# Performance work log

Measured on AMD Instinct MI355X. Metric: run time of the kernel, lower is better.

Reference implementation:

```python
import jax, jax.numpy as jnp
import numpy as np

B, T, HID = 2, 2048, 1024
NH = 8
QK_DIM = 1024
V_DIM = 2048
SCALE_BASE = 512.0
GN_EPS = 1e-5


def _xpos_rotate(x, downscale):
    # x: [B, T, QK_DIM]; XPOS rotary embedding (syncdoth/RetNet, offset=0)
    d = QK_DIM
    dh = d // 2
    pos = jnp.arange(T, dtype=jnp.float32)
    # per-pair magnitude scale
    base_scale = (jnp.arange(0, d, 2, dtype=jnp.float32) + 0.4 * d) / (1.4 * d)  # [dh]
    scale = base_scale[None, :] ** (pos[:, None] / SCALE_BASE)  # [T, dh]
    if downscale:
        scale = 1.0 / scale
    inv_freq = 1.0 / (10000.0 ** (jnp.arange(dh, dtype=jnp.float32) / dh))
    sinusoid = pos[:, None] * inv_freq[None, :]  # [T, dh]
    sin = jnp.sin(sinusoid) * scale
    cos = jnp.cos(sinusoid) * scale
    # duplicate_interleave -> [T, d]
    sin = jnp.repeat(sin, 2, axis=-1)
    cos = jnp.repeat(cos, 2, axis=-1)
    x1 = x[..., 0::2]
    x2 = x[..., 1::2]
    rot = jnp.stack((-x2, x1), axis=-1).reshape(x.shape)  # rotate_every_two
    return x * cos[None] + rot * sin[None]


def setup_inputs() -> dict:
    key = jax.random.key(0)
    k1, k2, k3, k4 = jax.random.split(key, 4)
    x = jax.random.normal(k1, (B, T, HID), dtype=jnp.float32)
    Wqkv = jax.random.normal(k2, (HID, 2 * QK_DIM + V_DIM), dtype=jnp.float32) / np.sqrt(HID)
    Wg = jax.random.normal(k3, (HID, V_DIM), dtype=jnp.float32) / np.sqrt(HID)
    Wp = jax.random.normal(k4, (V_DIM, HID), dtype=jnp.float32) / np.sqrt(V_DIM)
    bp = jnp.zeros((HID,), dtype=jnp.float32)
    return {"x": x, "Wqkv": Wqkv, "Wg": Wg, "Wp": Wp, "bp": bp}


def reference(x, Wqkv, Wg, Wp, bp):
    # multi-scale decay (non-default gamma path)
    gamma = 1.0 - jnp.exp(jnp.linspace(np.log(1.0 / 32), np.log(1.0 / 512), NH)).astype(jnp.float32)  # [NH]

    qkv = x @ Wqkv  # [B,T,2qk+v]
    q, k, v = jnp.split(qkv, [QK_DIM, 2 * QK_DIM], axis=-1)
    q = _xpos_rotate(q, downscale=False)
    k = _xpos_rotate(k, downscale=True)

    dqk = QK_DIM // NH
    dv = V_DIM // NH
    q = q.reshape(B, T, NH, dqk).transpose(0, 2, 1, 3)  # [B,H,T,dqk]
    k = k.reshape(B, T, NH, dqk).transpose(0, 2, 1, 3)
    v = v.reshape(B, T, NH, dv).transpose(0, 2, 1, 3)   # [B,H,T,dv]

    # parallel decay mask: gamma^(i-j) for i>=j else 0  -> [H,T,T]
    idx = jnp.arange(T)
    expo = idx[:, None] - idx[None, :]
    expo_safe = jnp.where(expo >= 0, expo, 0).astype(jnp.float32)
    decay_mask = jnp.where(expo[None] >= 0, gamma[:, None, None] ** expo_safe[None], 0.0)  # [H,T,T]

    scores = jnp.einsum('bhid,bhjd->bhij', q, k) * (dqk ** -0.5)
    retention = jnp.einsum('bhij,bhjv->bhiv', scores * decay_mask[None], v)  # [B,H,T,dv]

    # current_kv state: sum_t decay_mask[h,-1,t] * k_t (outer) v_t  -> [B,H,dqk,dv]
    curr_kv = jnp.einsum('bhtk,bhtv,ht->bhkv', k, v, decay_mask[:, -1, :])

    ret = retention.transpose(0, 2, 1, 3).reshape(B, T, V_DIM)

    # GroupNorm(num_groups=NH, affine=False) over [B*T, V_DIM]
    g = ret.reshape(B, T, NH, dv)
    mu = jnp.mean(g, axis=-1, keepdims=True)
    var = jnp.var(g, axis=-1, keepdims=True)
    normed = ((g - mu) / jnp.sqrt(var + GN_EPS)).reshape(B, T, V_DIM)

    gate = jax.nn.silu(x @ Wg)
    out = (gate * normed) @ Wp + bp
    return out, curr_kv
```

## Files before the change

kernel.cpp:

```cpp
#include <hip/hip_runtime.h>

typedef unsigned short u16;
typedef unsigned int   u32;
typedef unsigned long long u64;

typedef __attribute__((ext_vector_type(8))) short bf8_t;
typedef __attribute__((ext_vector_type(4))) float f4_t;

#define DEVI __device__ __forceinline__
#define MFMA16(a,b,c) __builtin_amdgcn_mfma_f32_16x16x32_bf16((a),(b),(c),0,0,0)

#define BB   2
#define TT   2048
#define HIDN 1024
#define L0f  (-3.4657359027997265f)
#define DLf  (-0.3960841031714215f)
#define SCL  (0.08838834764831845f)

DEVI u16 f2b(float f) {
    u32 u = __float_as_uint(f);
    u += 0x7FFFu + ((u >> 16) & 1u);
    return (u16)(u >> 16);
}
DEVI float b2f(u16 u) { return __uint_as_float(((u32)u) << 16); }

DEVI void gll16(const void* g, void* l) {
    __builtin_amdgcn_global_load_lds((const __attribute__((address_space(1))) void*)g,
                                     (__attribute__((address_space(3))) void*)l, 16, 0, 0);
}

__global__ __launch_bounds__(256) void k_tables(u32* __restrict__ cqp, u32* __restrict__ ckp,
                                                float* __restrict__ gt, float* __restrict__ gk) {
    int bx = blockIdx.x;
    if (bx >= 4096) {
        int i = (bx - 4096) * 256 + threadIdx.x;
        if (i < 16384) {
            int h = i >> 11, t = i & 2047;
            float lg2 = log2f(1.f - expf(L0f + (float)h * DLf));
            gt[i] = exp2f((float)(2047 - t) * lg2);
        } else {
            int idx = i - 16384;
            int h = idx >> 6, d = idx & 63;
            float lg2 = log2f(1.f - expf(L0f + (float)h * DLf));
            gk[idx] = exp2f(-(float)d * lg2);
        }
        return;
    }
    int idx = bx * 256 + threadIdx.x;
    int t = idx >> 9, m = idx & 511;
    float base = (2.f * (float)m + 409.6f) * (1.f / 1433.6f);
    float s = exp2f(log2f(base) * ((float)t * (1.f / 512.f)));
    float invf = exp2f(-(float)m * (13.287712379549449f / 512.f));
    float sn, cs;
    sincosf((float)t * invf, &sn, &cs);
    int h = m >> 6;
    float lg2h = log2f(1.f - expf(L0f + (float)h * DLf));
    float qf = s * SCL * exp2f((float)(t & 63) * lg2h);
    cqp[idx] = (u32)f2b(cs * qf) | ((u32)f2b(sn * qf) << 16);
    float is = 1.f / s;
    ckp[idx] = (u32)f2b(cs * is) | ((u32)f2b(sn * is) << 16);
}

__global__ __launch_bounds__(256) void k_cvt(const float* __restrict__ in, u16* __restrict__ out) {
    int i = blockIdx.x * 256 + threadIdx.x;
    float4 v = ((const float4*)in)[i];
    u64 pk = (u64)f2b(v.x) | ((u64)f2b(v.y) << 16) | ((u64)f2b(v.z) << 32) | ((u64)f2b(v.w) << 48);
    ((u64*)out)[i] = pk;
}

__global__ __launch_bounds__(256) void k_tposeF(const float* __restrict__ Wqkv,
                                                const float* __restrict__ Wg,
                                                const float* __restrict__ Wp,
                                                u16* __restrict__ oQ, u16* __restrict__ oG,
                                                u16* __restrict__ oP) {
    __shared__ float tile[32][33];
    int bx = blockIdx.x;
    const float* in; u16* out; int R, C, cx, ry;
    if (bx < 4096)      { in = Wqkv; out = oQ; R = 1024; C = 4096; cx = bx & 127;        ry = bx >> 7; }
    else if (bx < 6144) { int b2 = bx - 4096; in = Wg; out = oG; R = 1024; C = 2048; cx = b2 & 63; ry = b2 >> 6; }
    else                { int b2 = bx - 6144; in = Wp; out = oP; R = 2048; C = 1024; cx = b2 & 31; ry = b2 >> 5; }
    int c0 = cx * 32, r0 = ry * 32;
    int tx = threadIdx.x, ty = threadIdx.y;
#pragma unroll
    for (int i = 0; i < 4; i++)
        tile[ty * 4 + i][tx] = in[(size_t)(r0 + ty * 4 + i) * C + c0 + tx];
    __syncthreads();
#pragma unroll
    for (int i = 0; i < 4; i++)
        out[(size_t)(c0 + ty * 4 + i) * R + r0 + tx] = f2b(tile[tx][ty * 4 + i]);
}

DEVI void stage_tile(const u16* __restrict__ A, const u16* __restrict__ B,
                     int m0, int n0, int kt, char* buf, int tid, int wid) {
#pragma unroll
    for (int q = 0; q < 4; q++) {
        int flat = q * 8192 + tid * 16;
        int row = flat >> 7, byt = (flat & 127) ^ ((row & 7) << 4);
        gll16((const char*)A + (size_t)(m0 + row) * 2048 + kt * 128 + byt,
              buf + q * 8192 + wid * 1024);
        gll16((const char*)B + (size_t)(n0 + row) * 2048 + kt * 128 + byt,
              buf + 32768 + q * 8192 + wid * 1024);
    }
}

#define QPHASE(kk, fmh, LOADB)                                                        \
    {                                                                                 \
        bf8_t a_[4];                                                                  \
        _Pragma("unroll")                                                             \
        for (int f = 0; f < 4; f++) {                                                 \
            int ra = 128 * wr + ((fmh) * 4 + f) * 16 + lr;                            \
            a_[f] = *(const bf8_t*)(bA + ra * 128 + (((kk) * 64 + lg * 16) ^ ((ra & 7) << 4))); \
        }                                                                             \
        if (LOADB) {                                                                  \
            _Pragma("unroll")                                                         \
            for (int f = 0; f < 4; f++) {                                             \
                int rb = 64 * wc + f * 16 + lr;                                       \
                breg[f] = *(const bf8_t*)(bB + rb * 128 + (((kk) * 64 + lg * 16) ^ ((rb & 7) << 4))); \
            }                                                                         \
        }                                                                             \
        __builtin_amdgcn_s_barrier();                                                 \
        __builtin_amdgcn_s_setprio(1);                                                \
        _Pragma("unroll")                                                             \
        for (int f = 0; f < 4; f++)                                                   \
            _Pragma("unroll")                                                         \
            for (int j = 0; j < 4; j++)                                               \
                acc[(fmh) * 4 + f][j] = MFMA16(a_[f], breg[j], acc[(fmh) * 4 + f][j]); \
        __builtin_amdgcn_s_setprio(0);                                                \
        __builtin_amdgcn_s_barrier();                                                 \
    }

__global__ __launch_bounds__(512, 2) void k_gemm_qkvg8(
    const u16* __restrict__ xb, const u16* __restrict__ Wcat,
    const u32* __restrict__ cqp, const u32* __restrict__ ckp, const float* __restrict__ gkt,
    u16* __restrict__ qw, u16* __restrict__ kw, u16* __restrict__ kT, u16* __restrict__ vT,
    u16* __restrict__ gateb) {
    __shared__ __align__(16) char L[131072];
    int flat = blockIdx.x;
    int swz = (flat & 7) * 48 + (flat >> 3);
    int m0 = (swz / 24) * 256, n0 = (swz % 24) * 256;
    int tid = threadIdx.x, lane = tid & 63, wid = tid >> 6;
    int wr = wid >> 2, wc = wid & 3, lr = lane & 15, lg = lane >> 4;
    f4_t acc[8][4];
#pragma unroll
    for (int i = 0; i < 8; i++)
#pragma unroll
        for (int j = 0; j < 4; j++)
#pragma unroll
            for (int e = 0; e < 4; e++) acc[i][j][e] = 0.f;
    stage_tile(xb, Wcat, m0, n0, 0, L, tid, wid);
    __syncthreads();
    for (int kt = 0; kt < 16; ++kt) {
        const char* bA = L + (kt & 1) * 65536;
        const char* bB = bA + 32768;
        if (kt < 15) stage_tile(xb, Wcat, m0, n0, kt + 1, L + ((kt + 1) & 1) * 65536, tid, wid);
        bf8_t breg[4];
        QPHASE(0, 0, 1)
        QPHASE(0, 1, 0)
        QPHASE(1, 0, 1)
        QPHASE(1, 1, 0)
        __syncthreads();
    }
    char* SP = L;
    int b = m0 >> 11, t0 = m0 & 2047;
    if (n0 < 4096 && n0 >= 2048) {
        int h = (n0 - 2048) >> 8;
#pragma unroll
        for (int fm = 0; fm < 8; fm++)
#pragma unroll
            for (int fn = 0; fn < 4; fn++) {
                int dv = wc * 64 + fn * 16 + lr;
                int rowb = wr * 128 + fm * 16 + lg * 4;
                u64 pk = 0;
#pragma unroll
                for (int r = 0; r < 4; r++) pk |= ((u64)f2b(acc[fm][fn][r])) << (16 * r);
                *(u64*)(SP + dv * 512 + ((rowb * 2) ^ ((dv & 15) << 4))) = pk;
            }
        __syncthreads();
#pragma unroll
        for (int it = 0; it < 16; it++) {
            int chunk = it * 512 + tid;
            int dv = chunk >> 5, j = chunk & 31;
            uint4 v = *(const uint4*)(SP + dv * 512 + ((j * 16) ^ ((dv & 15) << 4)));
            *(uint4*)(vT + ((size_t)((b * 8 + h) * 256 + dv)) * 2048 + t0 + j * 8) = v;
        }
    } else if (n0 < 2048) {
        int isK = n0 >= 1024;
        const u32* cT = isK ? ckp : cqp;
        int hb = (n0 >> 7) & 7;
#pragma unroll
        for (int fm = 0; fm < 8; fm++)
#pragma unroll
            for (int fn = 0; fn < 4; fn++) {
                int col = wc * 64 + fn * 16 + lr;
                int gq = (n0 & 1023) + col;
                int mi = gq >> 1, h = gq >> 7;
                u64 pk = 0;
#pragma unroll
                for (int r = 0; r < 4; r++) {
                    int rowl = wr * 128 + fm * 16 + lg * 4 + r;
                    int t = t0 + rowl;
                    float v = acc[fm][fn][r];
                    float pv = __shfl_xor(v, 1);
                    u32 cp = cT[t * 512 + mi];
                    float cs = b2f((u16)cp), sn = b2f((u16)(cp >> 16));
                    float o = (col & 1) ? (v * cs + pv * sn) : (v * cs - pv * sn);
                    if (isK) {
                        pk |= ((u64)f2b(o)) << (16 * r);
                        o *= gkt[h * 64 + (t & 63)];
                    }
                    *(u16*)(SP + rowl * 512 + ((col * 2) ^ ((rowl & 15) << 4))) = f2b(o);
                }
                if (isK)
                    *(u64*)&kT[((size_t)((b * 8 + h) * 128 + (gq & 127))) * 2048 + t0 + wr * 128 + fm * 16 + lg * 4] = pk;
            }
        __syncthreads();
#pragma unroll
        for (int it = 0; it < 16; it++) {
            int chunk = it * 512 + tid;
            int r = chunk >> 5, j = chunk & 31;
            uint4 v = *(const uint4*)(SP + r * 512 + ((j * 16) ^ ((r & 15) << 4)));
            int hh = hb + (j >> 4);
            u16* g = (isK ? kw : qw) + ((size_t)((b * 8 + hh) * 2048 + t0 + r)) * 128 + (j & 15) * 8;
            *(uint4*)g = v;
        }
    } else {
        int c0 = n0 - 4096;
#pragma unroll
        for (int fm = 0; fm < 8; fm++)
#pragma unroll
            for (int fn = 0; fn < 4; fn++) {
                int col = wc * 64 + fn * 16 + lr;
#pragma unroll
                for (int r = 0; r < 4; r++) {
                    int rowl = wr * 128 + fm * 16 + lg * 4 + r;
                    float gg = acc[fm][fn][r];
                    *(u16*)(SP + rowl * 512 + ((col * 2) ^ ((rowl & 15) << 4))) = f2b(gg / (1.f + expf(-gg)));
                }
            }
        __syncthreads();
#pragma unroll
        for (int it = 0; it < 16; it++) {
            int chunk = it * 512 + tid;
            int r = chunk >> 5, j = chunk & 31;
            uint4 v = *(const uint4*)(SP + r * 512 + ((j * 16) ^ ((r & 15) << 4)));
            *(uint4*)(gateb + (size_t)(b * 2048 + t0 + r) * 2048 + c0 + j * 8) = v;
        }
    }
}

DEVI void gemm_ml(const u16* __restrict__ Ag, const u16* __restrict__ Bg, int Klen, int Kstr,
                  int m0, int n0, u16* As, u16* Bs, f4_t acc[4][4]) {
    int tid = threadIdx.x, lane = tid & 63, wid = tid >> 6;
    int wr = wid >> 1, wc = wid & 1, lr = lane & 15, lg = lane >> 4;
    for (int k0 = 0; k0 < Klen; k0 += 64) {
        __syncthreads();
#pragma unroll
        for (int p = 0; p < 4; p++) {
            int flat = p * 4096 + tid * 16;
            int row = flat >> 7, byt = (flat & 127) ^ ((row & 7) << 4);
            gll16((const char*)Ag + ((size_t)(m0 + row) * Kstr + k0) * 2 + byt,
                  (char*)As + p * 4096 + wid * 1024);
            gll16((const char*)Bg + ((size_t)(n0 + row) * Kstr + k0) * 2 + byt,
                  (char*)Bs + p * 4096 + wid * 1024);
        }
        __syncthreads();
#pragma unroll
        for (int kk = 0; kk < 2; kk++) {
            bf8_t a[4], b[4];
#pragma unroll
            for (int f = 0; f < 4; f++) {
                int ra = wr * 64 + f * 16 + lr;
                a[f] = *(const bf8_t*)((const char*)As + ra * 128 + ((kk * 64 + lg * 16) ^ ((ra & 7) << 4)));
                int rb = wc * 64 + f * 16 + lr;
                b[f] = *(const bf8_t*)((const char*)Bs + rb * 128 + ((kk * 64 + lg * 16) ^ ((rb & 7) << 4)));
            }
#pragma unroll
            for (int i = 0; i < 4; i++)
#pragma unroll
                for (int j = 0; j < 4; j++)
                    acc[i][j] = MFMA16(a[i], b[j], acc[i][j]);
        }
    }
}

DEVI void acc_zero(f4_t acc[4][4]) {
#pragma unroll
    for (int i = 0; i < 4; i++)
#pragma unroll
        for (int j = 0; j < 4; j++)
#pragma unroll
            for (int e = 0; e < 4; e++) acc[i][j][e] = 0.f;
}

__global__ __launch_bounds__(256) void k_gemm_outp(const u16* __restrict__ gdb, const u16* __restrict__ Wt,
                                                   float* __restrict__ part) {
    __shared__ u16 SM[128 * 128];
    f4_t acc[4][4]; acc_zero(acc);
    int m0 = blockIdx.y * 128, n0 = blockIdx.x * 128, kz = blockIdx.z;
    gemm_ml(gdb + kz * 1024, Wt + kz * 1024, 1024, 2048, m0, n0, SM, SM + 128 * 64, acc);
    int tid = threadIdx.x, lane = tid & 63, wid = tid >> 6;
    int wr = wid >> 1, wc = wid & 1, lr = lane & 15, lg = lane >> 4;
    float* SMf = (float*)SM;
    float* po = part + (size_t)kz * 4096 * 1024;
    __syncthreads();
#pragma unroll
    for (int p = 0; p < 2; p++) {
        if (p) __syncthreads();
        if (wr == p) {
#pragma unroll
            for (int fm = 0; fm < 4; fm++)
#pragma unroll
                for (int fn = 0; fn < 4; fn++) {
                    int col = wc * 64 + fn * 16 + lr;
#pragma unroll
                    for (int r = 0; r < 4; r++) {
                        int rowl = fm * 16 + lg * 4 + r;
                        *(float*)((char*)SMf + rowl * 512 + ((col * 4) ^ ((rowl & 7) << 6))) = acc[fm][fn][r];
                    }
                }
        }
        __syncthreads();
#pragma unroll
        for (int it2 = 0; it2 < 8; it2++) {
            int chunk = it2 * 256 + tid;
            int rowl = chunk >> 5, j = chunk & 31;
            f4_t v = *(const f4_t*)((const char*)SMf + rowl * 512 + ((j * 16) ^ ((rowl & 7) << 6)));
            *(f4_t*)((char*)po + ((size_t)(m0 + p * 64 + rowl) * 1024 + n0) * 4 + j * 16) = v;
        }
    }
}

__global__ __launch_bounds__(256) void k_outred(const float* __restrict__ part, const float* __restrict__ bp,
                                                float* __restrict__ outp) {
    int i = blockIdx.x * 256 + threadIdx.x;
    f4_t a = ((const f4_t*)part)[i];
    f4_t c = ((const f4_t*)(part + (size_t)4096 * 1024))[i];
    f4_t bb = *(const f4_t*)(bp + ((i * 4) & 1023));
#pragma unroll
    for (int e = 0; e < 4; e++) a[e] += c[e] + bb[e];
    ((f4_t*)outp)[i] = a;
}

__global__ __launch_bounds__(256, 3) void k_retention(const u16* __restrict__ qws, const u16* __restrict__ kws,
                                                      const u16* __restrict__ vTws,
                                                      u16* __restrict__ ret0, u16* __restrict__ ret1) {
    __shared__ u16 SMr[64 * 128 + 256 * 64];
    u16* Ks = SMr;
    u16* Vs = SMr + 64 * 128;
    int x = blockIdx.x;
    int it, jlo, jhi, toret1;
    if (x < 16)      { it = 15 - x;  jlo = 0;              jhi = it + 1;         toret1 = 0; }
    else if (x < 32) { it = x;       jlo = 0;              jhi = (it + 2) >> 1;  toret1 = 0; }
    else             { it = x - 16;  jlo = (it + 2) >> 1;  jhi = it + 1;         toret1 = 1; }
    int h = blockIdx.y, b = blockIdx.z;
    int bh = b * 8 + h;
    float lg2 = log2f(1.f - expf(L0f + (float)h * DLf));
    int i0 = it * 64;
    const u16* qbase = qws + (size_t)bh * 2048 * 128;
    const u16* kbase = kws + (size_t)bh * 2048 * 128;
    const u16* vbase = vTws + (size_t)bh * 256 * 2048;
    int tid = threadIdx.x, lane = tid & 63, w = tid >> 6, lr = lane & 15, lg = lane >> 4;
    bf8_t aq[4];
#pragma unroll
    for (int kk = 0; kk < 4; kk++)
        aq[kk] = *(const bf8_t*)((const char*)qbase + (size_t)(i0 + w * 16 + lr) * 256 + kk * 64 + lg * 16);
    f4_t racc[16];
#pragma unroll
    for (int f = 0; f < 16; f++)
#pragma unroll
        for (int e = 0; e < 4; e++) racc[f][e] = 0.f;
    for (int jt = jlo; jt < jhi; jt++) {
        int j0 = jt * 64;
        int diag = (jt == it);
        float tf = exp2f(64.f * (float)(it - jt) * lg2);
        __syncthreads();
#pragma unroll
        for (int p = 0; p < 4; p++) {
            int flat = p * 4096 + tid * 16;
            int row = flat >> 8, byt = (flat & 255) ^ ((row & 7) << 4);
            gll16((const char*)kbase + (size_t)(j0 + row) * 256 + byt, (char*)Ks + p * 4096 + w * 1024);
        }
#pragma unroll
        for (int p = 0; p < 8; p++) {
            int flat = p * 4096 + tid * 16;
            int row = flat >> 7, byt = (flat & 127) ^ ((row & 7) << 4);
            gll16((const char*)vbase + (size_t)row * 4096 + (size_t)j0 * 2 + byt,
                  (char*)Vs + p * 4096 + w * 1024);
        }
        __syncthreads();
        f4_t sacc[4];
#pragma unroll
        for (int f = 0; f < 4; f++)
#pragma unroll
            for (int e = 0; e < 4; e++) sacc[f][e] = 0.f;
#pragma unroll
        for (int kk = 0; kk < 4; kk++)
#pragma unroll
            for (int fn = 0; fn < 4; fn++) {
                int rb = fn * 16 + lr;
                bf8_t bb = *(const bf8_t*)((const char*)Ks + rb * 256 + ((kk * 64 + lg * 16) ^ ((rb & 7) << 4)));
                sacc[fn] = MFMA16(aq[kk], bb, sacc[fn]);
            }
        __syncthreads();
#pragma unroll
        for (int fn = 0; fn < 4; fn++)
#pragma unroll
            for (int r = 0; r < 4; r++) {
                int i_loc = w * 16 + lg * 4 + r;
                int col = fn * 16 + lr;
                float v = diag ? ((i_loc - col >= 0) ? sacc[fn][r] : 0.f) : sacc[fn][r] * tf;
                *(u16*)((char*)Ks + i_loc * 128 + ((col * 2) ^ ((i_loc & 7) << 4))) = f2b(v);
            }
#pragma unroll
        for (int kk = 0; kk < 2; kk++) {
            int ra = w * 16 + lr;
            bf8_t ap = *(const bf8_t*)((const char*)Ks + ra * 128 + ((kk * 64 + lg * 16) ^ ((ra & 7) << 4)));
#pragma unroll
            for (int fn2 = 0; fn2 < 16; fn2++) {
                int rb = fn2 * 16 + lr;
                bf8_t bv = *(const bf8_t*)((const char*)Vs + rb * 128 + ((kk * 64 + lg * 16) ^ ((rb & 7) << 4)));
                racc[fn2] = MFMA16(ap, bv, racc[fn2]);
            }
        }
    }
    __syncthreads();
    u16* St = Vs;
#pragma unroll
    for (int fn2 = 0; fn2 < 16; fn2++)
#pragma unroll
        for (int r = 0; r < 4; r++) {
            int il = w * 16 + lg * 4 + r;
            int dv = fn2 * 16 + lr;
            *(u16*)((char*)St + il * 512 + ((dv * 2) ^ ((il & 15) << 4))) = f2b(racc[fn2][r]);
        }
    __syncthreads();
#pragma unroll
    for (int it2 = 0; it2 < 8; it2++) {
        int chunk = it2 * 256 + tid;
        int il = chunk >> 5, j = chunk & 31;
        uint4 v = *(const uint4*)((const char*)St + il * 512 + ((j * 16) ^ ((il & 15) << 4)));
        char* dst;
        if (toret1) dst = (char*)ret1 + ((size_t)(b * 1024 + i0 - 1024 + il) * 2048 + h * 256) * 2 + j * 16;
        else        dst = (char*)ret0 + ((size_t)(b * 2048 + i0 + il) * 2048 + h * 256) * 2 + j * 16;
        *(uint4*)dst = v;
    }
}

__global__ __launch_bounds__(512) void k_currkv(const u16* __restrict__ kTws, const u16* __restrict__ vTws,
                                                const float* __restrict__ gtab, float* __restrict__ part) {
    __shared__ u16 Ks2[128 * 64];
    __shared__ u16 Vws[256 * 64];
    int tr = blockIdx.x;
    int bh = blockIdx.y;
    int h = bh & 7;
    const u16* kT = kTws + (size_t)bh * 128 * 2048;
    const u16* vT = vTws + (size_t)bh * 256 * 2048;
    const float* gt = gtab + h * 2048;
    int tid = threadIdx.x, lane = tid & 63, wid = tid >> 6;
    int wr = wid >> 2, wc = wid & 3, lr = lane & 15, lg = lane >> 4;
    f4_t acc[4][4]; acc_zero(acc);
    for (int tc = 0; tc < 8; tc++) {
        int t0 = tr * 512 + tc * 64;
        __syncthreads();
#pragma unroll
        for (int p = 0; p < 2; p++) {
            int flat = p * 8192 + tid * 16;
            int row = flat >> 7, byt = (flat & 127) ^ ((row & 7) << 4);
            gll16((const char*)kT + (size_t)row * 4096 + (size_t)t0 * 2 + byt,
                  (char*)Ks2 + p * 8192 + wid * 1024);
        }
#pragma unroll
        for (int p = 0; p < 4; p++) {
            int flat = p * 8192 + tid * 16;
            int row = flat >> 7, byt = flat & 127;
            int tt = t0 + (byt >> 1);
            const u16* src = vT + (size_t)row * 2048 + tt;
            u16 tmp[8]; *(uint4*)tmp = *(const uint4*)src;
            const float* gp = gt + tt;
            u16 op[8];
#pragma unroll
            for (int e = 0; e < 8; e++) op[e] = f2b(b2f(tmp[e]) * gp[e]);
            *(uint4*)((char*)Vws + row * 128 + (byt ^ ((row & 7) << 4))) = *(uint4*)op;
        }
        __syncthreads();
#pragma unroll
        for (int kk = 0; kk < 2; kk++) {
            bf8_t a[4], bb[4];
#pragma unroll
            for (int f = 0; f < 4; f++) {
                int ra = wr * 64 + f * 16 + lr;
                a[f] = *(const bf8_t*)((const char*)Ks2 + ra * 128 + ((kk * 64 + lg * 16) ^ ((ra & 7) << 4)));
                int rb = wc * 64 + f * 16 + lr;
                bb[f] = *(const bf8_t*)((const char*)Vws + rb * 128 + ((kk * 64 + lg * 16) ^ ((rb & 7) << 4)));
            }
#pragma unroll
            for (int i = 0; i < 4; i++)
#pragma unroll
                for (int j = 0; j < 4; j++)
                    acc[i][j] = MFMA16(a[i], bb[j], acc[i][j]);
        }
    }
#pragma unroll
    for (int fm = 0; fm < 4; fm++)
#pragma unroll
        for (int fn = 0; fn < 4; fn++)
#pragma unroll
            for (int r = 0; r < 4; r++) {
                int dk = wr * 64 + fm * 16 + lg * 4 + r;
                int dv = wc * 64 + fn * 16 + lr;
                part[((size_t)(bh * 4 + tr)) * 32768 + (size_t)dk * 256 + dv] = acc[fm][fn][r];
            }
}

__global__ __launch_bounds__(256) void k_reduce_ckv(const float* __restrict__ part, float* __restrict__ outc) {
    int i = blockIdx.x * 256 + threadIdx.x;
    int bh = i >> 15, wv = i & 32767;
    float s = 0.f;
#pragma unroll
    for (int tr = 0; tr < 4; tr++) s += part[((size_t)(bh * 4 + tr)) * 32768 + wv];
    outc[i] = s;
}

__global__ __launch_bounds__(256) void k_gnorm(const u16* __restrict__ ret0, const u16* __restrict__ ret1,
                                               const u16* __restrict__ gateb, u16* __restrict__ gatedb) {
    int g = blockIdx.x * 4 + (threadIdx.x >> 6);
    int lane = threadIdx.x & 63;
    int row = g >> 3, h = g & 7;
    size_t base = (size_t)row * 2048 + h * 256 + lane * 4;
    u64 p0 = *(const u64*)(ret0 + base);
    float e0 = b2f((u16)p0), e1 = b2f((u16)(p0 >> 16)), e2 = b2f((u16)(p0 >> 32)), e3 = b2f((u16)(p0 >> 48));
    if ((row & 2047) >= 1024) {
        size_t b1 = (size_t)((row >> 11) * 1024 + (row & 1023)) * 2048 + h * 256 + lane * 4;
        u64 p1 = *(const u64*)(ret1 + b1);
        e0 += b2f((u16)p1); e1 += b2f((u16)(p1 >> 16)); e2 += b2f((u16)(p1 >> 32)); e3 += b2f((u16)(p1 >> 48));
    }
    float s = e0 + e1 + e2 + e3;
    float sqs = e0 * e0 + e1 * e1 + e2 * e2 + e3 * e3;
#pragma unroll
    for (int m = 1; m < 64; m <<= 1) { s += __shfl_xor(s, m); sqs += __shfl_xor(sqs, m); }
    float mean = s * (1.f / 256.f);
    float var = sqs * (1.f / 256.f) - mean * mean;
    float inv = rsqrtf(var + 1e-5f);
    u64 gp = *(const u64*)(gateb + base);
    u64 pk = (u64)f2b((e0 - mean) * inv * b2f((u16)gp)) |
             ((u64)f2b((e1 - mean) * inv * b2f((u16)(gp >> 16))) << 16) |
             ((u64)f2b((e2 - mean) * inv * b2f((u16)(gp >> 32))) << 32) |
             ((u64)f2b((e3 - mean) * inv * b2f((u16)(gp >> 48))) << 48);
    *(u64*)(gatedb + base) = pk;
}

extern "C" void kernel_launch(void* const* d_in, const int* in_sizes, int n_in,
                              void* d_out, int out_size, void* d_ws, size_t ws_size,
                              hipStream_t stream) {
    const float* x    = (const float*)d_in[0];
    const float* Wqkv = (const float*)d_in[1];
    const float* Wg   = (const float*)d_in[2];
    const float* Wp   = (const float*)d_in[3];
    const float* bp   = (const float*)d_in[4];
    float* outp   = (float*)d_out;
    float* outckv = outp + (size_t)BB * TT * HIDN;

    char* ws = (char*)d_ws;
    const size_t MB = 1024 * 1024;
    u16*   xb     = (u16*)(ws);
    u16*   WqkvT  = (u16*)(ws + 8 * MB);
    u16*   WgT    = (u16*)(ws + 16 * MB);
    u16*   WpT    = (u16*)(ws + 20 * MB);
    u32*   cqp    = (u32*)(ws + 24 * MB);
    u32*   ckp    = (u32*)(ws + 28 * MB);
    u16*   gateb  = (u16*)(ws + 32 * MB);
    u16*   qw     = (u16*)(ws + 48 * MB);
    u16*   kw     = (u16*)(ws + 56 * MB);
    u16*   kT     = (u16*)(ws + 64 * MB);
    u16*   vT     = (u16*)(ws + 72 * MB);
    u16*   ret0b  = (u16*)(ws + 88 * MB);
    u16*   ret1b  = (u16*)(ws + 104 * MB);
    float* ckvp   = (float*)(ws + 112 * MB);
    float* gtab   = (float*)(ws + 120 * MB);
    float* gkt    = (float*)(ws + 120 * MB + 65536);
    u16*   gatedb = (u16*)(ws + 48 * MB);
    float* opart  = (float*)(ws + 88 * MB);

    hipLaunchKernelGGL(k_tables, dim3(4162), dim3(256), 0, stream, cqp, ckp, gtab, gkt);
    hipLaunchKernelGGL(k_cvt, dim3(4096), dim3(256), 0, stream, x, xb);
    hipLaunchKernelGGL(k_tposeF, dim3(8192), dim3(32, 8), 0, stream, Wqkv, Wg, Wp, WqkvT, WgT, WpT);
    hipLaunchKernelGGL(k_gemm_qkvg8, dim3(384), dim3(512), 0, stream,
                       xb, WqkvT, cqp, ckp, gkt, qw, kw, kT, vT, gateb);
    hipLaunchKernelGGL(k_currkv, dim3(4, 16), dim3(512), 0, stream, kT, vT, gtab, ckvp);
    hipLaunchKernelGGL(k_reduce_ckv, dim3(2048), dim3(256), 0, stream, ckvp, outckv);
    hipLaunchKernelGGL(k_retention, dim3(48, 8, 2), dim3(256), 0, stream, qw, kw, vT, ret0b, ret1b);
    hipLaunchKernelGGL(k_gnorm, dim3(8192), dim3(256), 0, stream, ret0b, ret1b, gateb, gatedb);
    hipLaunchKernelGGL(k_gemm_outp, dim3(8, 32, 2), dim3(256), 0, stream, gatedb, WpT, opart);
    hipLaunchKernelGGL(k_outred, dim3(4096), dim3(256), 0, stream, opart, bp, outp);
}
```

Measured before the change: 225.4 us.

## Halve QKVG GEMM K-tile to 32 to cut LDS and raise occupancy

The fused QKV/gate GEMM now stages K-tiles of 32 instead of 64 (64 KB of LDS instead of 128 KB), doubling the k-loop count. Launch bounds change from 2 to 4 blocks per CU. The epilogues are split into two passes, one per warp-row half, so they fit in the smaller shared buffer. The goal is more resident blocks to hide latency, at the cost of more barriers per k step and an extra epilogue barrier. With 512 threads and a 32-float4 accumulator array per thread, register pressure may limit the actual occupancy gain.

```diff
diff --git a/kernel.cpp b/kernel.cpp
--- a/kernel.cpp
+++ b/kernel.cpp
@@ -90,32 +90,32 @@
         out[(size_t)(c0 + ty * 4 + i) * R + r0 + tx] = f2b(tile[tx][ty * 4 + i]);
 }
 
-DEVI void stage_tile(const u16* __restrict__ A, const u16* __restrict__ B,
-                     int m0, int n0, int kt, char* buf, int tid, int wid) {
-#pragma unroll
-    for (int q = 0; q < 4; q++) {
-        int flat = q * 8192 + tid * 16;
-        int row = flat >> 7, byt = (flat & 127) ^ ((row & 7) << 4);
-        gll16((const char*)A + (size_t)(m0 + row) * 2048 + kt * 128 + byt,
-              buf + q * 8192 + wid * 1024);
-        gll16((const char*)B + (size_t)(n0 + row) * 2048 + kt * 128 + byt,
-              buf + 32768 + q * 8192 + wid * 1024);
-    }
-}
-
-#define QPHASE(kk, fmh, LOADB)                                                        \
+DEVI void stage32(const u16* __restrict__ A, const u16* __restrict__ B,
+                  int m0, int n0, int kt, char* buf, int lane, int wid) {
+#pragma unroll
+    for (int q = 0; q < 2; q++) {
+        int flat = (wid * 2 + q) * 1024 + lane * 16;
+        int row = flat >> 6, byt = (flat & 63) ^ ((row & 3) << 4);
+        gll16((const char*)A + (size_t)(m0 + row) * 2048 + kt * 64 + byt,
+              buf + (wid * 2 + q) * 1024);
+        gll16((const char*)B + (size_t)(n0 + row) * 2048 + kt * 64 + byt,
+              buf + 16384 + (wid * 2 + q) * 1024);
+    }
+}
+
+#define QPHASE32(fmh, LOADB)                                                          \
     {                                                                                 \
         bf8_t a_[4];                                                                  \
         _Pragma("unroll")                                                             \
         for (int f = 0; f < 4; f++) {                                                 \
             int ra = 128 * wr + ((fmh) * 4 + f) * 16 + lr;                            \
-            a_[f] = *(const bf8_t*)(bA + ra * 128 + (((kk) * 64 + lg * 16) ^ ((ra & 7) << 4))); \
+            a_[f] = *(const bf8_t*)(bA + ra * 64 + ((lg * 16) ^ ((ra & 3) << 4)));    \
         }                                                                             \
         if (LOADB) {                                                                  \
             _Pragma("unroll")                                                         \
             for (int f = 0; f < 4; f++) {                                             \
                 int rb = 64 * wc + f * 16 + lr;                                       \
-                breg[f] = *(const bf8_t*)(bB + rb * 128 + (((kk) * 64 + lg * 16) ^ ((rb & 7) << 4))); \
+                breg[f] = *(const bf8_t*)(bB + rb * 64 + ((lg * 16) ^ ((rb & 3) << 4))); \
             }                                                                         \
         }                                                                             \
         __builtin_amdgcn_s_barrier();                                                 \
@@ -129,12 +129,12 @@
         __builtin_amdgcn_s_barrier();                                                 \
     }
 
-__global__ __launch_bounds__(512, 2) void k_gemm_qkvg8(
+__global__ __launch_bounds__(512, 4) void k_gemm_qkvg8(
     const u16* __restrict__ xb, const u16* __restrict__ Wcat,
     const u32* __restrict__ cqp, const u32* __restrict__ ckp, const float* __restrict__ gkt,
     u16* __restrict__ qw, u16* __restrict__ kw, u16* __restrict__ kT, u16* __restrict__ vT,
     u16* __restrict__ gateb) {
-    __shared__ __align__(16) char L[131072];
+    __shared__ __align__(16) char L[65536];
     int flat = blockIdx.x;
     int swz = (flat & 7) * 48 + (flat >> 3);
     int m0 = (swz / 24) * 256, n0 = (swz % 24) * 256;
@@ -147,103 +147,119 @@
         for (int j = 0; j < 4; j++)
 #pragma unroll
             for (int e = 0; e < 4; e++) acc[i][j][e] = 0.f;
-    stage_tile(xb, Wcat, m0, n0, 0, L, tid, wid);
+    stage32(xb, Wcat, m0, n0, 0, L, lane, wid);
     __syncthreads();
-    for (int kt = 0; kt < 16; ++kt) {
-        const char* bA = L + (kt & 1) * 65536;
-        const char* bB = bA + 32768;
-        if (kt < 15) stage_tile(xb, Wcat, m0, n0, kt + 1, L + ((kt + 1) & 1) * 65536, tid, wid);
+    for (int kt = 0; kt < 32; ++kt) {
+        const char* bA = L + (kt & 1) * 32768;
+        const char* bB = bA + 16384;
+        if (kt < 31) stage32(xb, Wcat, m0, n0, kt + 1, L + ((kt + 1) & 1) * 32768, lane, wid);
         bf8_t breg[4];
-        QPHASE(0, 0, 1)
-        QPHASE(0, 1, 0)
-        QPHASE(1, 0, 1)
-        QPHASE(1, 1, 0)
+        QPHASE32(0, 1)
+        QPHASE32(1, 0)
         __syncthreads();
     }
     char* SP = L;
     int b = m0 >> 11, t0 = m0 & 2047;
-    if (n0 < 4096 && n0 >= 2048) {
+    if (n0 >= 2048 && n0 < 4096) {
         int h = (n0 - 2048) >> 8;
 #pragma unroll
-        for (int fm = 0; fm < 8; fm++)
-#pragma unroll
-            for (int fn = 0; fn < 4; fn++) {
-                int dv = wc * 64 + fn * 16 + lr;
-                int rowb = wr * 128 + fm * 16 + lg * 4;
-                u64 pk = 0;
-#pragma unroll
-                for (int r = 0; r < 4; r++) pk |= ((u64)f2b(acc[fm][fn][r])) << (16 * r);
-                *(u64*)(SP + dv * 512 + ((rowb * 2) ^ ((dv & 15) << 4))) = pk;
-            }
-        __syncthreads();
-#pragma unroll
-        for (int it = 0; it < 16; it++) {
-            int chunk = it * 512 + tid;
-            int dv = chunk >> 5, j = chunk & 31;
-            uint4 v = *(const uint4*)(SP + dv * 512 + ((j * 16) ^ ((dv & 15) << 4)));
-            *(uint4*)(vT + ((size_t)((b * 8 + h) * 256 + dv)) * 2048 + t0 + j * 8) = v;
+        for (int p = 0; p < 2; p++) {
+            if (p) __syncthreads();
+            if (wr == p) {
+#pragma unroll
+                for (int fm = 0; fm < 8; fm++)
+#pragma unroll
+                    for (int fn = 0; fn < 4; fn++) {
+                        int dv = wc * 64 + fn * 16 + lr;
+                        int tl = fm * 16 + lg * 4;
+                        u64 pk = 0;
+#pragma unroll
+                        for (int r = 0; r < 4; r++) pk |= ((u64)f2b(acc[fm][fn][r])) << (16 * r);
+                        *(u64*)(SP + dv * 256 + ((tl * 2) ^ ((dv & 15) << 4))) = pk;
+                    }
+            }
+            __syncthreads();
+#pragma unroll
+            for (int it = 0; it < 8; it++) {
+                int chunk = it * 512 + tid;
+                int dv = chunk >> 4, j = chunk & 15;
+                uint4 v = *(const uint4*)(SP + dv * 256 + ((j * 16) ^ ((dv & 15) << 4)));
+                *(uint4*)(vT + ((size_t)((b * 8 + h) * 256 + dv)) * 2048 + t0 + p * 128 + j * 8) = v;
+            }
         }
     } else if (n0 < 2048) {
         int isK = n0 >= 1024;
         const u32* cT = isK ? ckp : cqp;
         int hb = (n0 >> 7) & 7;
 #pragma unroll
-        for (int fm = 0; fm < 8; fm++)
-#pragma unroll
-            for (int fn = 0; fn < 4; fn++) {
-                int col = wc * 64 + fn * 16 + lr;
-                int gq = (n0 & 1023) + col;
-                int mi = gq >> 1, h = gq >> 7;
-                u64 pk = 0;
-#pragma unroll
-                for (int r = 0; r < 4; r++) {
-                    int rowl = wr * 128 + fm * 16 + lg * 4 + r;
-                    int t = t0 + rowl;
-                    float v = acc[fm][fn][r];
-                    float pv = __shfl_xor(v, 1);
-                    u32 cp = cT[t * 512 + mi];
-                    float cs = b2f((u16)cp), sn = b2f((u16)(cp >> 16));
-                    float o = (col & 1) ? (v * cs + pv * sn) : (v * cs - pv * sn);
-                    if (isK) {
-                        pk |= ((u64)f2b(o)) << (16 * r);
-                        o *= gkt[h * 64 + (t & 63)];
+        for (int p = 0; p < 2; p++) {
+            if (p) __syncthreads();
+            if (wr == p) {
+#pragma unroll
+                for (int fm = 0; fm < 8; fm++)
+#pragma unroll
+                    for (int fn = 0; fn < 4; fn++) {
+                        int col = wc * 64 + fn * 16 + lr;
+                        int gq = (n0 & 1023) + col;
+                        int mi = gq >> 1, h = gq >> 7;
+                        u64 pk = 0;
+#pragma unroll
+                        for (int r = 0; r < 4; r++) {
+                            int rowl = fm * 16 + lg * 4 + r;
+                            int t = t0 + p * 128 + rowl;
+                            float v = acc[fm][fn][r];
+                            float pv = __shfl_xor(v, 1);
+                            u32 cp = cT[t * 512 + mi];
+                            float cs = b2f((u16)cp), sn = b2f((u16)(cp >> 16));
+                            float o = (col & 1) ? (v * cs + pv * sn) : (v * cs - pv * sn);
+                            if (isK) {
+                                pk |= ((u64)f2b(o)) << (16 * r);
+                                o *= gkt[h * 64 + (t & 63)];
+                            }
+                            *(u16*)(SP + rowl * 512 + ((col * 2) ^ ((rowl & 15) << 4))) = f2b(o);
+                        }
+                        if (isK)
+                            *(u64*)&kT[((size_t)((b * 8 + h) * 128 + (gq & 127))) * 2048 + t0 + p * 128 + fm * 16 + lg * 4] = pk;
                     }
-                    *(u16*)(SP + rowl * 512 + ((col * 2) ^ ((rowl & 15) << 4))) = f2b(o);
-                }
-                if (isK)
-                    *(u64*)&kT[((size_t)((b * 8 + h) * 128 + (gq & 127))) * 2048 + t0 + wr * 128 + fm * 16 + lg * 4] = pk;
-            }
-        __syncthreads();
-#pragma unroll
-        for (int it = 0; it < 16; it++) {
-            int chunk = it * 512 + tid;
-            int r = chunk >> 5, j = chunk & 31;
-            uint4 v = *(const uint4*)(SP + r * 512 + ((j * 16) ^ ((r & 15) << 4)));
-            int hh = hb + (j >> 4);
-            u16* g = (isK ? kw : qw) + ((size_t)((b * 8 + hh) * 2048 + t0 + r)) * 128 + (j & 15) * 8;
-            *(uint4*)g = v;
+            }
+            __syncthreads();
+#pragma unroll
+            for (int it = 0; it < 8; it++) {
+                int chunk = it * 512 + tid;
+                int r = chunk >> 5, j = chunk & 31;
+                uint4 v = *(const uint4*)(SP + r * 512 + ((j * 16) ^ ((r & 15) << 4)));
+                int hh = hb + (j >> 4);
+                u16* g = (isK ? kw : qw) + ((size_t)((b * 8 + hh) * 2048 + t0 + p * 128 + r)) * 128 + (j & 15) * 8;
+                *(uint4*)g = v;
+            }
         }
     } else {
         int c0 = n0 - 4096;
 #pragma unroll
-        for (int fm = 0; fm < 8; fm++)
-#pragma unroll
-            for (int fn = 0; fn < 4; fn++) {
-                int col = wc * 64 + fn * 16 + lr;
-#pragma unroll
-                for (int r = 0; r < 4; r++) {
-                    int rowl = wr * 128 + fm * 16 + lg * 4 + r;
-                    float gg = acc[fm][fn][r];
-                    *(u16*)(SP + rowl * 512 + ((col * 2) ^ ((rowl & 15) << 4))) = f2b(gg / (1.f + expf(-gg)));
-                }
-            }
-        __syncthreads();
-#pragma unroll
-        for (int it = 0; it < 16; it++) {
-            int chunk = it * 512 + tid;
-            int r = chunk >> 5, j = chunk & 31;
-            uint4 v = *(const uint4*)(SP + r * 512 + ((j * 16) ^ ((r & 15) << 4)));
-            *(uint4*)(gateb + (size_t)(b * 2048 + t0 + r) * 2048 + c0 + j * 8) = v;
+        for (int p = 0; p < 2; p++) {
+            if (p) __syncthreads();
+            if (wr == p) {
+#pragma unroll
+                for (int fm = 0; fm < 8; fm++)
+#pragma unroll
+                    for (int fn = 0; fn < 4; fn++) {
+                        int col = wc * 64 + fn * 16 + lr;
+#pragma unroll
+                        for (int r = 0; r < 4; r++) {
+                            int rowl = fm * 16 + lg * 4 + r;
+                            float gg = acc[fm][fn][r];
+                            *(u16*)(SP + rowl * 512 + ((col * 2) ^ ((rowl & 15) << 4))) = f2b(gg / (1.f + expf(-gg)));
+                        }
+                    }
+            }
+            __syncthreads();
+#pragma unroll
+            for (int it = 0; it < 8; it++) {
+                int chunk = it * 512 + tid;
+                int r = chunk >> 5, j = chunk & 31;
+                uint4 v = *(const uint4*)(SP + r * 512 + ((j * 16) ^ ((r & 15) << 4)));
+                *(uint4*)(gateb + (size_t)(b * 2048 + t0 + p * 128 + r) * 2048 + c0 + j * 8) = v;
+            }
         }
     }
 }
```

New measurement: 668.8 us. +196.8%, slower.
